# Performance work log

Measured on AMD Instinct MI355X. Metric: run time of the kernel, lower is better.

## Reference

```python
import jax, jax.numpy as jnp
import numpy as np

N_EMBD = 1024
N_HEAD = 16
HEAD_SIZE = N_EMBD // N_HEAD
B, T = 2, 2048
LN_EPS = 1e-5


def _layernorm(x, g, b):
    mu = jnp.mean(x, axis=-1, keepdims=True)
    var = jnp.var(x, axis=-1, keepdims=True)
    return (x - mu) * jax.lax.rsqrt(var + LN_EPS) * g + b


def setup_inputs() -> dict:
    key = jax.random.key(0)
    ks = jax.random.split(key, 12)
    s_in = 1.0 / np.sqrt(N_EMBD)
    s_ff = 1.0 / np.sqrt(4 * N_EMBD)
    return {
        "x": jax.random.normal(ks[0], (B, T, N_EMBD), jnp.float32),
        # per-head q/k/v linears stacked head-major: [n_embd, n_embd]
        "Wq": jax.random.uniform(ks[1], (N_EMBD, N_EMBD), jnp.float32, -s_in, s_in),
        "Wk": jax.random.uniform(ks[2], (N_EMBD, N_EMBD), jnp.float32, -s_in, s_in),
        "Wv": jax.random.uniform(ks[3], (N_EMBD, N_EMBD), jnp.float32, -s_in, s_in),
        "Wo": jax.random.uniform(ks[4], (N_EMBD, N_EMBD), jnp.float32, -s_in, s_in),
        "bo": jax.random.uniform(ks[5], (N_EMBD,), jnp.float32, -s_in, s_in),
        "W1": jax.random.uniform(ks[6], (N_EMBD, 4 * N_EMBD), jnp.float32, -s_in, s_in),
        "b1": jax.random.uniform(ks[7], (4 * N_EMBD,), jnp.float32, -s_in, s_in),
        "W2": jax.random.uniform(ks[8], (4 * N_EMBD, N_EMBD), jnp.float32, -s_ff, s_ff),
        "b2": jax.random.uniform(ks[9], (N_EMBD,), jnp.float32, -s_ff, s_ff),
        "g1": jnp.ones((N_EMBD,), jnp.float32),
        "be1": jnp.zeros((N_EMBD,), jnp.float32),
        "g2": jnp.ones((N_EMBD,), jnp.float32),
        "be2": jnp.zeros((N_EMBD,), jnp.float32),
    }


def reference(x, Wq, Wk, Wv, Wo, bo, W1, b1, W2, b2, g1, be1, g2, be2):
    Bx, Tx, C = x.shape
    # --- self-attention on ln1(x) ---
    h = _layernorm(x, g1, be1)
    q = (h @ Wq).reshape(Bx, Tx, N_HEAD, HEAD_SIZE)
    k = (h @ Wk).reshape(Bx, Tx, N_HEAD, HEAD_SIZE)
    v = (h @ Wv).reshape(Bx, Tx, N_HEAD, HEAD_SIZE)
    # NOTE: faithful to source -- scale uses full C (n_embd), not head_size
    scale = C ** (-0.5)
    wei = jnp.einsum("bqhd,bkhd->bhqk", q, k) * scale  # [B,H,T,T]
    causal = jnp.tril(jnp.ones((Tx, Tx), bool))
    wei = jnp.where(causal, wei, -jnp.inf)
    wei = jax.nn.softmax(wei, axis=-1)
    attn = jnp.einsum("bhqk,bkhd->bqhd", wei, v).reshape(Bx, Tx, C)
    x = x + (attn @ Wo + bo)
    # --- feed-forward on ln2(x) ---
    h2 = _layernorm(x, g2, be2)
    x = x + (jax.nn.relu(h2 @ W1 + b1) @ W2 + b2)
    return x
```

## Files before the change

kernel.cpp:

```cpp
#include <hip/hip_runtime.h>
#include <hip/hip_bf16.h>
#include <math.h>

#define BB 2
#define TT 2048
#define CC 1024
#define NH 16
#define HD 64
#define BT (BB*TT)
#define LN_EPS 1e-5f
#define ATT_SCALE 0.03125f

typedef __bf16 bf16x8 __attribute__((ext_vector_type(8)));
typedef __bf16 bf16x4 __attribute__((ext_vector_type(4)));
typedef short shortx4 __attribute__((ext_vector_type(4)));
typedef float floatx4 __attribute__((ext_vector_type(4)));

__device__ __forceinline__ void gl_lds16(const __bf16* g, __bf16* l) {
    __builtin_amdgcn_global_load_lds((const __attribute__((address_space(1))) void*)g,
                                     (__attribute__((address_space(3))) void*)l,
                                     16, 0, 0);
}

#define MFMA32(a, b, c) __builtin_amdgcn_mfma_f32_16x16x32_bf16(a, b, c, 0, 0, 0)

#if __has_builtin(__builtin_amdgcn_mfma_f32_16x16x16_bf16)
__device__ __forceinline__ floatx4 mfma16(bf16x4 a, bf16x4 b, floatx4 c) {
    return __builtin_amdgcn_mfma_f32_16x16x16_bf16(a, b, c, 0, 0, 0);
}
#else
__device__ __forceinline__ floatx4 mfma16(bf16x4 a, bf16x4 b, floatx4 c) {
    return __builtin_amdgcn_mfma_f32_16x16x16bf16_1k(
        __builtin_bit_cast(shortx4, a), __builtin_bit_cast(shortx4, b), c, 0, 0, 0);
}
#endif

__global__ __launch_bounds__(256) void ln_kernel(const float* __restrict__ x,
                                                 const float* __restrict__ g,
                                                 const float* __restrict__ b,
                                                 __bf16* __restrict__ out) {
    int row = blockIdx.x;
    const float4* xr = (const float4*)(x + (size_t)row * CC);
    float4 v = xr[threadIdx.x];
    float s  = v.x + v.y + v.z + v.w;
    float ss = v.x*v.x + v.y*v.y + v.z*v.z + v.w*v.w;
    #pragma unroll
    for (int off = 32; off; off >>= 1) {
        s  += __shfl_down(s, off);
        ss += __shfl_down(ss, off);
    }
    __shared__ float rs_[4], rss_[4];
    __shared__ float mu_s, inv_s;
    int lane = threadIdx.x & 63, wid = threadIdx.x >> 6;
    if (lane == 0) { rs_[wid] = s; rss_[wid] = ss; }
    __syncthreads();
    if (threadIdx.x == 0) {
        float S  = rs_[0] + rs_[1] + rs_[2] + rs_[3];
        float SS = rss_[0] + rss_[1] + rss_[2] + rss_[3];
        float mu  = S * (1.0f / CC);
        float var = SS * (1.0f / CC) - mu * mu;
        mu_s  = mu;
        inv_s = rsqrtf(var + LN_EPS);
    }
    __syncthreads();
    float mu = mu_s, inv = inv_s;
    float4 gv = ((const float4*)g)[threadIdx.x];
    float4 bv = ((const float4*)b)[threadIdx.x];
    bf16x4 o;
    o[0] = (__bf16)((v.x - mu) * inv * gv.x + bv.x);
    o[1] = (__bf16)((v.y - mu) * inv * gv.y + bv.y);
    o[2] = (__bf16)((v.z - mu) * inv * gv.z + bv.z);
    o[3] = (__bf16)((v.w - mu) * inv * gv.w + bv.w);
    *(bf16x4*)(out + (size_t)row * CC + threadIdx.x * 4) = o;
}

__global__ __launch_bounds__(256) void transpose_all(
        const float* __restrict__ Wq, const float* __restrict__ Wk,
        const float* __restrict__ Wv, const float* __restrict__ Wo,
        const float* __restrict__ W1, const float* __restrict__ W2,
        __bf16* __restrict__ WqkvT, __bf16* __restrict__ WoT,
        __bf16* __restrict__ W1T, __bf16* __restrict__ W2T) {
    int idx = blockIdx.x;
    const float* src; __bf16* dst; int K, N, tn, tk;
    if (idx < 3072) {
        int wsel = idx >> 10, local = idx & 1023;
        src = (wsel == 0) ? Wq : (wsel == 1 ? Wk : Wv);
        dst = WqkvT + (size_t)wsel * 1024 * 1024;
        K = 1024; N = 1024; tn = local & 31; tk = local >> 5;
    } else if (idx < 4096) {
        int local = idx - 3072;
        src = Wo; dst = WoT; K = 1024; N = 1024; tn = local & 31; tk = local >> 5;
    } else if (idx < 8192) {
        int local = idx - 4096;
        src = W1; dst = W1T; K = 1024; N = 4096; tn = local & 127; tk = local >> 7;
    } else {
        int local = idx - 8192;
        src = W2; dst = W2T; K = 4096; N = 1024; tn = local & 31; tk = local >> 5;
    }
    __shared__ float t[32][33];
    int n0 = tn * 32, k0 = tk * 32;
    int tx = threadIdx.x & 31, ty = threadIdx.x >> 5;
    #pragma unroll
    for (int r = ty; r < 32; r += 8)
        t[r][tx] = src[(size_t)(k0 + r) * N + n0 + tx];
    __syncthreads();
    #pragma unroll
    for (int r = ty; r < 32; r += 8)
        dst[(size_t)(n0 + r) * K + k0 + tx] = (__bf16)t[tx][r];
}

template<int NT, typename OT, bool BIAS, bool RELU, bool RES, bool VSPLIT>
__global__ __launch_bounds__(256) void gemm_bf16(const __bf16* __restrict__ A,
                                                 const __bf16* __restrict__ Bt,
                                                 const float* __restrict__ bias,
                                                 const float* __restrict__ res,
                                                 OT* __restrict__ C,
                                                 __bf16* __restrict__ vt,
                                                 int M, int N, int K) {
    constexpr int JN = NT / 32;
    __shared__ __bf16 As[128 * 32];
    __shared__ __bf16 Bs[NT * 32];
    const int tid = threadIdx.x;
    const int l = tid & 63, w = tid >> 6;
    const int m = l & 15, g = l >> 4;
    const int wm = w >> 1, wn = w & 1;
    const int m0 = blockIdx.y * 128, n0 = blockIdx.x * NT;

    const int srow = w * 16 + (l >> 2);
    const int skof = (l & 3) * 8;
    const __bf16* ga = A  + (size_t)(m0 + srow) * K + skof;
    const __bf16* gb = Bt + (size_t)(n0 + srow) * K + skof;
    __bf16* la0 = As + w * 512;
    __bf16* lb0 = Bs + w * 512;

    floatx4 acc[4][JN];
    #pragma unroll
    for (int i = 0; i < 4; ++i)
        #pragma unroll
        for (int j = 0; j < JN; ++j) {
            floatx4 z = {0.f, 0.f, 0.f, 0.f};
            acc[i][j] = z;
        }

    for (int kt = 0; kt < K; kt += 32) {
        __syncthreads();
        gl_lds16(ga,                  la0);
        gl_lds16(ga + (size_t)64 * K, la0 + 2048);
        gl_lds16(gb,                  lb0);
        if (NT == 128)
            gl_lds16(gb + (size_t)64 * K, lb0 + 2048);
        ga += 32; gb += 32;
        __syncthreads();

        bf16x8 af[4], bfr[JN];
        #pragma unroll
        for (int i = 0; i < 4; ++i)
            af[i] = *(const bf16x8*)&As[(wm * 64 + i * 16 + m) * 32 + g * 8];
        #pragma unroll
        for (int j = 0; j < JN; ++j)
            bfr[j] = *(const bf16x8*)&Bs[(wn * (NT / 2) + j * 16 + m) * 32 + g * 8];
        #pragma unroll
        for (int i = 0; i < 4; ++i)
            #pragma unroll
            for (int j = 0; j < JN; ++j)
                acc[i][j] = MFMA32(af[i], bfr[j], acc[i][j]);
    }

    if (VSPLIT && n0 >= 2048) {
        #pragma unroll
        for (int i = 0; i < 4; ++i) {
            int row = m0 + wm * 64 + i * 16 + g * 4;
            int bb = row >> 11, t0 = row & 2047;
            #pragma unroll
            for (int j = 0; j < JN; ++j) {
                int cv = n0 + wn * (NT / 2) + j * 16 + m - 2048;
                bf16x4 o;
                #pragma unroll
                for (int r = 0; r < 4; ++r) o[r] = (__bf16)acc[i][j][r];
                *(bf16x4*)(vt + ((size_t)(bb * NH + (cv >> 6)) * HD + (cv & 63)) * 2048 + t0) = o;
            }
        }
    } else {
        #pragma unroll
        for (int i = 0; i < 4; ++i) {
            int row = m0 + wm * 64 + i * 16 + g * 4;
            #pragma unroll
            for (int j = 0; j < JN; ++j) {
                int col = n0 + wn * (NT / 2) + j * 16 + m;
                float bv = BIAS ? bias[col] : 0.0f;
                #pragma unroll
                for (int r = 0; r < 4; ++r) {
                    float vo = acc[i][j][r] + bv;
                    if (RELU) vo = fmaxf(vo, 0.0f);
                    if (RES)  vo += res[(size_t)(row + r) * N + col];
                    C[(size_t)(row + r) * N + col] = (OT)vo;
                }
            }
        }
    }
}

__global__ __launch_bounds__(256, 2) void attn_mfma2(const __bf16* __restrict__ qkv,
                                                     const __bf16* __restrict__ vt,
                                                     __bf16* __restrict__ att) {
    const int qt = 15 - (int)blockIdx.x;
    const int h = blockIdx.y, b = blockIdx.z;
    const int tid = threadIdx.x;
    const int l = tid & 63, w = tid >> 6;
    const int m = l & 15, g = l >> 4;

    __shared__ __bf16 Ks[2][128][32];
    __shared__ __bf16 Vt3[8][64][16];

    const __bf16* qp = qkv + (size_t)b * TT * 3072 + h * HD;
    const __bf16* kp = qp + 1024;
    const __bf16* vh = vt + (size_t)(b * NH + h) * HD * 2048;

    bf16x8 qb[2][2];
    #pragma unroll
    for (int nt = 0; nt < 2; ++nt) {
        int qrow = qt * 128 + w * 32 + nt * 16 + m;
        qb[nt][0] = *(const bf16x8*)(qp + (size_t)qrow * 3072 + g * 8);
        qb[nt][1] = *(const bf16x8*)(qp + (size_t)qrow * 3072 + 32 + g * 8);
    }

    floatx4 O[2][4];
    float m_s[2], l_s[2];
    #pragma unroll
    for (int nt = 0; nt < 2; ++nt) {
        #pragma unroll
        for (int jd = 0; jd < 4; ++jd) {
            floatx4 z = {0.f, 0.f, 0.f, 0.f};
            O[nt][jd] = z;
        }
        m_s[nt] = -1e30f; l_s[nt] = 0.0f;
    }

    for (int kt = 0; kt <= qt; ++kt) {
        __syncthreads();
        #pragma unroll
        for (int c = 0; c < 4; ++c) {
            int idx = w * 4 + c;
            int dh = idx >> 3, k16 = idx & 7;
            gl_lds16(kp + (size_t)(kt * 128 + k16 * 16 + (l >> 2)) * 3072 + dh * 32 + (l & 3) * 8,
                     (__bf16*)Ks + dh * 4096 + k16 * 512);
        }
        #pragma unroll
        for (int c = 0; c < 4; ++c) {
            int idx = w * 4 + c;
            int jt = idx >> 1, dhf = idx & 1;
            gl_lds16(vh + (size_t)(dhf * 32 + (l >> 1)) * 2048 + kt * 128 + jt * 16 + (l & 1) * 8,
                     (__bf16*)Vt3 + jt * 1024 + dhf * 512);
        }
        __syncthreads();

        floatx4 S[2][8];
        #pragma unroll
        for (int jt = 0; jt < 8; ++jt) {
            bf16x8 kf0 = *(const bf16x8*)&Ks[0][jt * 16 + m][g * 8];
            bf16x8 kf1 = *(const bf16x8*)&Ks[1][jt * 16 + m][g * 8];
            #pragma unroll
            for (int nt = 0; nt < 2; ++nt) {
                floatx4 z = {0.f, 0.f, 0.f, 0.f};
                z = MFMA32(kf0, qb[nt][0], z);
                S[nt][jt] = MFMA32(kf1, qb[nt][1], z);
            }
        }

        bf16x4 pv[2][8];
        const bool last = (kt == qt);
        #pragma unroll
        for (int nt = 0; nt < 2; ++nt) {
            if (last) {
                int qr = w * 32 + nt * 16 + m;
                #pragma unroll
                for (int jt = 0; jt < 8; ++jt)
                    #pragma unroll
                    for (int r = 0; r < 4; ++r)
                        if (jt * 16 + g * 4 + r > qr) S[nt][jt][r] = -1e30f;
            }
            float mx = -1e30f;
            #pragma unroll
            for (int jt = 0; jt < 8; ++jt)
                #pragma unroll
                for (int r = 0; r < 4; ++r)
                    mx = fmaxf(mx, S[nt][jt][r]);
            mx = fmaxf(mx, __shfl_xor(mx, 16, 64));
            mx = fmaxf(mx, __shfl_xor(mx, 32, 64));
            float mnew = fmaxf(m_s[nt], mx);
            float alpha = __expf((m_s[nt] - mnew) * ATT_SCALE);
            m_s[nt] = mnew;
            float mc = mnew * ATT_SCALE;
            float ls = 0.0f;
            #pragma unroll
            for (int jt = 0; jt < 8; ++jt) {
                bf16x4 t;
                #pragma unroll
                for (int r = 0; r < 4; ++r) {
                    float p = __expf(fmaf(S[nt][jt][r], ATT_SCALE, -mc));
                    ls += p;
                    t[r] = (__bf16)p;
                }
                pv[nt][jt] = t;
            }
            ls += __shfl_xor(ls, 16, 64);
            ls += __shfl_xor(ls, 32, 64);
            l_s[nt] = l_s[nt] * alpha + ls;
            #pragma unroll
            for (int jd = 0; jd < 4; ++jd) O[nt][jd] *= alpha;
        }

        #pragma unroll
        for (int jt = 0; jt < 8; ++jt)
            #pragma unroll
            for (int jd = 0; jd < 4; ++jd) {
                bf16x4 vf = *(const bf16x4*)&Vt3[jt][jd * 16 + m][g * 4];
                #pragma unroll
                for (int nt = 0; nt < 2; ++nt)
                    O[nt][jd] = mfma16(vf, pv[nt][jt], O[nt][jd]);
            }
    }

    #pragma unroll
    for (int nt = 0; nt < 2; ++nt) {
        float inv = 1.0f / l_s[nt];
        int qrow = qt * 128 + w * 32 + nt * 16 + m;
        #pragma unroll
        for (int jd = 0; jd < 4; ++jd) {
            bf16x4 o;
            #pragma unroll
            for (int r = 0; r < 4; ++r) o[r] = (__bf16)(O[nt][jd][r] * inv);
            *(bf16x4*)(att + ((size_t)b * TT + qrow) * CC + h * HD + jd * 16 + g * 4) = o;
        }
    }
}

extern "C" void kernel_launch(void* const* d_in, const int* in_sizes, int n_in,
                              void* d_out, int out_size, void* d_ws, size_t ws_size,
                              hipStream_t stream) {
    const float* x   = (const float*)d_in[0];
    const float* Wq  = (const float*)d_in[1];
    const float* Wk  = (const float*)d_in[2];
    const float* Wv  = (const float*)d_in[3];
    const float* Wo  = (const float*)d_in[4];
    const float* bo  = (const float*)d_in[5];
    const float* W1  = (const float*)d_in[6];
    const float* b1  = (const float*)d_in[7];
    const float* W2  = (const float*)d_in[8];
    const float* b2  = (const float*)d_in[9];
    const float* g1  = (const float*)d_in[10];
    const float* be1 = (const float*)d_in[11];
    const float* g2  = (const float*)d_in[12];
    const float* be2 = (const float*)d_in[13];
    float* out = (float*)d_out;

    char* p = (char*)d_ws;
    __bf16* hb    = (__bf16*)p; p += (size_t)BT * CC * 2;
    __bf16* qkvb  = (__bf16*)p; p += (size_t)BT * 3072 * 2;
    __bf16* vtb   = (__bf16*)p; p += (size_t)BT * CC * 2;
    __bf16* attb  = (__bf16*)p; p += (size_t)BT * CC * 2;
    float*  x2    = (float*)p;  p += (size_t)BT * CC * 4;
    __bf16* ffb   = (__bf16*)p; p += (size_t)BT * 4096 * 2;
    __bf16* WqkvT = (__bf16*)p; p += (size_t)3072 * 1024 * 2;
    __bf16* WoT   = (__bf16*)p; p += (size_t)1024 * 1024 * 2;
    __bf16* W1T   = (__bf16*)p; p += (size_t)4096 * 1024 * 2;
    __bf16* W2T   = (__bf16*)p; p += (size_t)1024 * 4096 * 2;

    transpose_all<<<12288, 256, 0, stream>>>(Wq, Wk, Wv, Wo, W1, W2,
                                             WqkvT, WoT, W1T, W2T);
    ln_kernel<<<BT, 256, 0, stream>>>(x, g1, be1, hb);
    gemm_bf16<128, __bf16, false, false, false, true><<<dim3(24, 32), 256, 0, stream>>>(
        hb, WqkvT, nullptr, nullptr, qkvb, vtb, BT, 3072, 1024);
    attn_mfma2<<<dim3(16, NH, BB), 256, 0, stream>>>(qkvb, vtb, attb);
    gemm_bf16<64, float, true, false, true, false><<<dim3(16, 32), 256, 0, stream>>>(
        attb, WoT, bo, x, x2, nullptr, BT, 1024, 1024);
    ln_kernel<<<BT, 256, 0, stream>>>(x2, g2, be2, hb);
    gemm_bf16<128, __bf16, true, true, false, false><<<dim3(32, 32), 256, 0, stream>>>(
        hb, W1T, b1, nullptr, ffb, nullptr, BT, 4096, 1024);
    gemm_bf16<64, float, true, false, true, false><<<dim3(16, 32), 256, 0, stream>>>(
        ffb, W2T, b2, x2, out, nullptr, BT, 1024, 4096);
}
```

Baseline: 398.9 us.

## Split-K the Wo and W2 GEMMs with fused reduce plus residual and LayerNorm

Adds a split-K option to the bf16 GEMM, which writes bf16 partial sums into a pooled scratch buffer. The Wo projection uses 2-way split-K and the W2 projection uses 4-way split-K with 128-wide tiles. New row-wise reduction kernels add the partials, bias and residual, and the Wo reduction also applies LayerNorm 2, replacing the separate ln_kernel launch. The goal is more blocks in flight for the narrow N=1024 GEMMs. The cost is extra partial-sum traffic and the precision loss of storing partials in bf16.

```diff
diff --git a/kernel.cpp b/kernel.cpp
--- a/kernel.cpp
+++ b/kernel.cpp
@@ -72,6 +72,76 @@
     o[2] = (__bf16)((v.z - mu) * inv * gv.z + bv.z);
     o[3] = (__bf16)((v.w - mu) * inv * gv.w + bv.w);
     *(bf16x4*)(out + (size_t)row * CC + threadIdx.x * 4) = o;
+}
+
+__global__ __launch_bounds__(256) void reduce_wo_ln(const __bf16* __restrict__ P,
+                                                    const float* __restrict__ bo,
+                                                    const float* __restrict__ x,
+                                                    const float* __restrict__ g2,
+                                                    const float* __restrict__ be2,
+                                                    float* __restrict__ x2,
+                                                    __bf16* __restrict__ hb) {
+    int row = blockIdx.x;
+    int c = threadIdx.x * 4;
+    bf16x4 a0 = *(const bf16x4*)(P + (size_t)row * CC + c);
+    bf16x4 a1 = *(const bf16x4*)(P + (size_t)BT * CC + (size_t)row * CC + c);
+    float4 xb = *(const float4*)(x + (size_t)row * CC + c);
+    float4 bb = *(const float4*)(bo + c);
+    float4 v;
+    v.x = xb.x + bb.x + (float)a0[0] + (float)a1[0];
+    v.y = xb.y + bb.y + (float)a0[1] + (float)a1[1];
+    v.z = xb.z + bb.z + (float)a0[2] + (float)a1[2];
+    v.w = xb.w + bb.w + (float)a0[3] + (float)a1[3];
+    *(float4*)(x2 + (size_t)row * CC + c) = v;
+
+    float s  = v.x + v.y + v.z + v.w;
+    float ss = v.x*v.x + v.y*v.y + v.z*v.z + v.w*v.w;
+    #pragma unroll
+    for (int off = 32; off; off >>= 1) {
+        s  += __shfl_down(s, off);
+        ss += __shfl_down(ss, off);
+    }
+    __shared__ float rs_[4], rss_[4];
+    __shared__ float mu_s, inv_s;
+    int lane = threadIdx.x & 63, wid = threadIdx.x >> 6;
+    if (lane == 0) { rs_[wid] = s; rss_[wid] = ss; }
+    __syncthreads();
+    if (threadIdx.x == 0) {
+        float S  = rs_[0] + rs_[1] + rs_[2] + rs_[3];
+        float SS = rss_[0] + rss_[1] + rss_[2] + rss_[3];
+        float mu  = S * (1.0f / CC);
+        float var = SS * (1.0f / CC) - mu * mu;
+        mu_s  = mu;
+        inv_s = rsqrtf(var + LN_EPS);
+    }
+    __syncthreads();
+    float mu = mu_s, inv = inv_s;
+    float4 gv = ((const float4*)g2)[threadIdx.x];
+    float4 bv = ((const float4*)be2)[threadIdx.x];
+    bf16x4 o;
+    o[0] = (__bf16)((v.x - mu) * inv * gv.x + bv.x);
+    o[1] = (__bf16)((v.y - mu) * inv * gv.y + bv.y);
+    o[2] = (__bf16)((v.z - mu) * inv * gv.z + bv.z);
+    o[3] = (__bf16)((v.w - mu) * inv * gv.w + bv.w);
+    *(bf16x4*)(hb + (size_t)row * CC + c) = o;
+}
+
+__global__ __launch_bounds__(256) void reduce_ffn(const __bf16* __restrict__ P,
+                                                  const float* __restrict__ b2,
+                                                  const float* __restrict__ x2,
+                                                  float* __restrict__ out) {
+    int row = blockIdx.x;
+    int c = threadIdx.x * 4;
+    const size_t S = (size_t)BT * CC;
+    float4 v = *(const float4*)(x2 + (size_t)row * CC + c);
+    float4 bb = *(const float4*)(b2 + c);
+    v.x += bb.x; v.y += bb.y; v.z += bb.z; v.w += bb.w;
+    #pragma unroll
+    for (int z = 0; z < 4; ++z) {
+        bf16x4 a = *(const bf16x4*)(P + z * S + (size_t)row * CC + c);
+        v.x += (float)a[0]; v.y += (float)a[1]; v.z += (float)a[2]; v.w += (float)a[3];
+    }
+    *(float4*)(out + (size_t)row * CC + c) = v;
 }
 
 __global__ __launch_bounds__(256) void transpose_all(
@@ -109,7 +179,7 @@
         dst[(size_t)(n0 + r) * K + k0 + tx] = (__bf16)t[tx][r];
 }
 
-template<int NT, typename OT, bool BIAS, bool RELU, bool RES, bool VSPLIT>
+template<int NT, int SK, typename OT, bool BIAS, bool RELU, bool RES, bool VSPLIT>
 __global__ __launch_bounds__(256) void gemm_bf16(const __bf16* __restrict__ A,
                                                  const __bf16* __restrict__ Bt,
                                                  const float* __restrict__ bias,
@@ -125,11 +195,13 @@
     const int m = l & 15, g = l >> 4;
     const int wm = w >> 1, wn = w & 1;
     const int m0 = blockIdx.y * 128, n0 = blockIdx.x * NT;
+    const int Keff = K / SK;
+    const int kbase = (SK > 1) ? (int)blockIdx.z * Keff : 0;
 
     const int srow = w * 16 + (l >> 2);
     const int skof = (l & 3) * 8;
-    const __bf16* ga = A  + (size_t)(m0 + srow) * K + skof;
-    const __bf16* gb = Bt + (size_t)(n0 + srow) * K + skof;
+    const __bf16* ga = A  + (size_t)(m0 + srow) * K + kbase + skof;
+    const __bf16* gb = Bt + (size_t)(n0 + srow) * K + kbase + skof;
     __bf16* la0 = As + w * 512;
     __bf16* lb0 = Bs + w * 512;
 
@@ -142,7 +214,7 @@
             acc[i][j] = z;
         }
 
-    for (int kt = 0; kt < K; kt += 32) {
+    for (int kt = 0; kt < Keff; kt += 32) {
         __syncthreads();
         gl_lds16(ga,                  la0);
         gl_lds16(ga + (size_t)64 * K, la0 + 2048);
@@ -166,7 +238,20 @@
                 acc[i][j] = MFMA32(af[i], bfr[j], acc[i][j]);
     }
 
-    if (VSPLIT && n0 >= 2048) {
+    if (SK > 1) {
+        __bf16* P = (__bf16*)C + (size_t)blockIdx.z * M * N;
+        #pragma unroll
+        for (int i = 0; i < 4; ++i) {
+            int row = m0 + wm * 64 + i * 16 + g * 4;
+            #pragma unroll
+            for (int j = 0; j < JN; ++j) {
+                int col = n0 + wn * (NT / 2) + j * 16 + m;
+                #pragma unroll
+                for (int r = 0; r < 4; ++r)
+                    P[(size_t)(row + r) * N + col] = (__bf16)acc[i][j][r];
+            }
+        }
+    } else if (VSPLIT && n0 >= 2048) {
         #pragma unroll
         for (int i = 0; i < 4; ++i) {
             int row = m0 + wm * 64 + i * 16 + g * 4;
@@ -355,10 +440,13 @@
     float* out = (float*)d_out;
 
     char* p = (char*)d_ws;
+    char*   pool  = p;          p += (size_t)32 * 1024 * 1024;
+    __bf16* qkvb  = (__bf16*)pool;
+    __bf16* vtb   = (__bf16*)(pool + (size_t)BT * 3072 * 2);
+    __bf16* wop   = (__bf16*)pool;
+    __bf16* ffp   = (__bf16*)pool;
+    __bf16* attb  = (__bf16*)p; p += (size_t)BT * CC * 2;
     __bf16* hb    = (__bf16*)p; p += (size_t)BT * CC * 2;
-    __bf16* qkvb  = (__bf16*)p; p += (size_t)BT * 3072 * 2;
-    __bf16* vtb   = (__bf16*)p; p += (size_t)BT * CC * 2;
-    __bf16* attb  = (__bf16*)p; p += (size_t)BT * CC * 2;
     float*  x2    = (float*)p;  p += (size_t)BT * CC * 4;
     __bf16* ffb   = (__bf16*)p; p += (size_t)BT * 4096 * 2;
     __bf16* WqkvT = (__bf16*)p; p += (size_t)3072 * 1024 * 2;
@@ -369,14 +457,15 @@
     transpose_all<<<12288, 256, 0, stream>>>(Wq, Wk, Wv, Wo, W1, W2,
                                              WqkvT, WoT, W1T, W2T);
     ln_kernel<<<BT, 256, 0, stream>>>(x, g1, be1, hb);
-    gemm_bf16<128, __bf16, false, false, false, true><<<dim3(24, 32), 256, 0, stream>>>(
+    gemm_bf16<128, 1, __bf16, false, false, false, true><<<dim3(24, 32), 256, 0, stream>>>(
         hb, WqkvT, nullptr, nullptr, qkvb, vtb, BT, 3072, 1024);
     attn_mfma2<<<dim3(16, NH, BB), 256, 0, stream>>>(qkvb, vtb, attb);
-    gemm_bf16<64, float, true, false, true, false><<<dim3(16, 32), 256, 0, stream>>>(
-        attb, WoT, bo, x, x2, nullptr, BT, 1024, 1024);
-    ln_kernel<<<BT, 256, 0, stream>>>(x2, g2, be2, hb);
-    gemm_bf16<128, __bf16, true, true, false, false><<<dim3(32, 32), 256, 0, stream>>>(
+    gemm_bf16<64, 2, __bf16, false, false, false, false><<<dim3(16, 32, 2), 256, 0, stream>>>(
+        attb, WoT, nullptr, nullptr, wop, nullptr, BT, 1024, 1024);
+    reduce_wo_ln<<<BT, 256, 0, stream>>>(wop, bo, x, g2, be2, x2, hb);
+    gemm_bf16<128, 1, __bf16, true, true, false, false><<<dim3(32, 32), 256, 0, stream>>>(
         hb, W1T, b1, nullptr, ffb, nullptr, BT, 4096, 1024);
-    gemm_bf16<64, float, true, false, true, false><<<dim3(16, 32), 256, 0, stream>>>(
-        ffb, W2T, b2, x2, out, nullptr, BT, 1024, 4096);
-}
+    gemm_bf16<128, 4, __bf16, false, false, false, false><<<dim3(8, 32, 4), 256, 0, stream>>>(
+        ffb, W2T, nullptr, nullptr, ffp, nullptr, BT, 1024, 4096);
+    reduce_ffn<<<BT, 256, 0, stream>>>(ffp, b2, x2, out);
+}
```

After: 397.0 us. Within noise of the previous version (-0.5%).
